# Performance work log

Measured on AMD Instinct MI355X. Metric: run time of the kernel, lower is better.

## Reference

```python
import jax, jax.numpy as jnp
import numpy as np
from jax.scipy.special import logsumexp

B, S, H, T = 64, 512, 768, 9

def setup_inputs() -> dict:
    key = jax.random.key(0)
    ks = jax.random.split(key, 6)
    return {
        "encoder_out": jax.random.normal(ks[0], (B, S, H), jnp.float32),
        "labels": jax.random.randint(ks[1], (B, S), 0, T, jnp.int32),
        "mask": jnp.ones((B, S), jnp.int32),
        "lengths": jnp.full((B,), S, jnp.int32),
        "fc_w": jax.random.normal(ks[2], (T, H), jnp.float32) * 0.02,
        "fc_b": jnp.zeros((T,), jnp.float32),
        "start_trans": jax.random.uniform(ks[3], (T,), jnp.float32, -0.1, 0.1),
        "end_trans": jax.random.uniform(ks[4], (T,), jnp.float32, -0.1, 0.1),
        "trans": jax.random.uniform(ks[5], (T, T), jnp.float32, -0.1, 0.1),
    }

def crf_log_likelihood(em, tg, mk, start, end, trans):
    # em: [S,B,T], tg: [S,B], mk: [S,B] float. torchcrf forward (reduction='none').
    barange = jnp.arange(em.shape[1])
    # --- numerator: score of the gold path ---
    score0 = start[tg[0]] + em[0][barange, tg[0]]
    def num_step(carry, x):
        score, prev = carry
        em_i, tg_i, mk_i = x
        score = score + (trans[prev, tg_i] + em_i[barange, tg_i]) * mk_i
        prev = jnp.where(mk_i > 0, tg_i, prev)
        return (score, prev), None
    (score, prev), _ = jax.lax.scan(num_step, (score0, tg[0]), (em[1:], tg[1:], mk[1:]))
    numerator = score + end[prev]
    # --- denominator: log partition via forward algorithm ---
    alpha = start[None, :] + em[0]  # [B,T]
    def den_step(alpha, x):
        em_i, mk_i = x
        nxt = logsumexp(alpha[:, :, None] + trans[None] + em_i[:, None, :], axis=1)
        return jnp.where(mk_i[:, None] > 0, nxt, alpha), None
    alpha, _ = jax.lax.scan(den_step, alpha, (em[1:], mk[1:]))
    denominator = logsumexp(alpha + end[None, :], axis=1)
    return numerator - denominator  # [B]

def crf_viterbi(em, mk, start, end, trans):
    # em: [S,B,T], mk: [S,B] float. Returns best path [S,B].
    barange = jnp.arange(em.shape[1])
    alpha = start[None, :] + em[0]  # [B,T]
    idT = jnp.arange(em.shape[2])[None, :]
    def fwd_step(alpha, x):
        em_i, mk_i = x
        scores = alpha[:, :, None] + trans[None]  # [B, T_prev, T_cur]
        bp = jnp.argmax(scores, axis=1)           # [B,T]
        nxt = jnp.max(scores, axis=1) + em_i
        valid = mk_i[:, None] > 0
        return jnp.where(valid, nxt, alpha), jnp.where(valid, bp, idT)
    alpha, bps = jax.lax.scan(fwd_step, alpha, (em[1:], mk[1:]))  # bps: [S-1,B,T]
    last = jnp.argmax(alpha + end[None, :], axis=1)  # [B]
    def back_step(tag, bp):
        prev = bp[barange, tag]
        return prev, prev
    _, path_head = jax.lax.scan(back_step, last, bps, reverse=True)  # [S-1,B]
    return jnp.concatenate([path_head, last[None, :]], axis=0)  # [S,B]

def reference(encoder_out, labels, mask, lengths, fc_w, fc_b, start_trans, end_trans, trans):
    # dropout in eval mode == identity
    emissions = jnp.einsum('bsh,th->bst', encoder_out, fc_w) + fc_b  # [B,S,T]
    em = jnp.swapaxes(emissions, 0, 1)               # [S,B,T]
    tg = jnp.swapaxes(labels, 0, 1)                  # [S,B]
    mk = jnp.swapaxes(mask, 0, 1).astype(emissions.dtype)
    ll = crf_log_likelihood(em, tg, mk, start_trans, end_trans, trans)  # [B]
    ner_loss = jnp.mean(-ll)
    path = crf_viterbi(em, mk, start_trans, end_trans, trans)  # [S,B]
    ner_predict = jnp.swapaxes(path, 0, 1)  # [B,S]
    return ner_loss, ner_predict, lengths
```

## Files before the change

### kernel.cpp

```cpp
#include <hip/hip_runtime.h>

#define Bsz 64
#define Ssz 512
#define Hsz 768
#define Tsz 9
#define NCH 16
#define LOG2E 1.4426950408889634f
#define LN2F  0.6931471805599453f
#define PSTR 17

__device__ __forceinline__ int SK(int s) { return s * Tsz + ((s >> 5) << 1); }

__global__ __launch_bounds__(256, 1) void emscan2_kernel(
    const float* __restrict__ x, const float* __restrict__ fcw,
    const float* __restrict__ fcb, const int* __restrict__ mask,
    const float* __restrict__ trans, float* __restrict__ em,
    float* __restrict__ R2, float* __restrict__ MV, int* __restrict__ cnt) {
    __shared__ __align__(16) float4 w4[Tsz * Hsz / 4];
    __shared__ float bias[Tsz];
    __shared__ float part[16 * Tsz * PSTR];
    __shared__ float em_w[33 * Tsz];
    __shared__ int   mk_w[33];
    __shared__ float Elds[81];
    __shared__ float Tlds[81];

    const int tid = threadIdx.x;
    const int bc = blockIdx.x;
    const int b = bc >> 4, c = bc & 15;
    const int base = c * 32;
    const size_t pos0 = (size_t)bc * 32;

    if (bc == 0 && tid == 0) *cnt = 0;

    const float4* fw4 = reinterpret_cast<const float4*>(fcw);
#pragma unroll
    for (int i = 0; i < 7; ++i) {
        const int o = tid + i * 256;
        if (o < 1728) w4[o] = fw4[o];
    }
    if (tid < Tsz) bias[tid] = fcb[tid];
    if (tid >= 16 && tid < 16 + 81) {
        const float t = trans[tid - 16];
        Tlds[tid - 16] = t;
        Elds[tid - 16] = exp2f(t * LOG2E);
    }
    if (tid >= 128 && tid < 128 + 33) {
        const int s = base + (tid - 128);
        mk_w[tid - 128] = (s < Ssz) ? mask[b * Ssz + s] : 0;
    }
    __syncthreads();

    const int p = tid >> 4, l = tid & 15;
    {
        const float4* xr0 = reinterpret_cast<const float4*>(x + (pos0 + p) * Hsz);
        const float4* xr1 = reinterpret_cast<const float4*>(x + (pos0 + 16 + p) * Hsz);
        float acc[Tsz][2];
#pragma unroll
        for (int t = 0; t < Tsz; ++t) { acc[t][0] = 0.0f; acc[t][1] = 0.0f; }
#pragma unroll 4
        for (int i = 0; i < 12; ++i) {
            const float4 xv0 = xr0[i * 16 + l];
            const float4 xv1 = xr1[i * 16 + l];
#pragma unroll
            for (int t = 0; t < Tsz; ++t) {
                const float4 wv = w4[t * 192 + i * 16 + l];
                acc[t][0] = fmaf(xv0.x, wv.x, fmaf(xv0.y, wv.y,
                            fmaf(xv0.z, wv.z, fmaf(xv0.w, wv.w, acc[t][0]))));
                acc[t][1] = fmaf(xv1.x, wv.x, fmaf(xv1.y, wv.y,
                            fmaf(xv1.z, wv.z, fmaf(xv1.w, wv.w, acc[t][1]))));
            }
        }
#pragma unroll
        for (int k = 0; k < 2; ++k) {
            __syncthreads();
#pragma unroll
            for (int t = 0; t < Tsz; ++t) part[(p * Tsz + t) * PSTR + l] = acc[t][k];
            __syncthreads();
            if (tid < 16 * Tsz) {
                const int pq = tid / Tsz, t = tid - pq * Tsz;
                float s = bias[t];
#pragma unroll
                for (int l2 = 0; l2 < 16; ++l2) s += part[(pq * Tsz + t) * PSTR + l2];
                em[(pos0 + (size_t)k * 16 + pq) * Tsz + t] = s;
                em_w[(k * 16 + pq) * Tsz + t] = s;
            }
        }
    }
    if (c < 15) {
        float acc2[Tsz];
#pragma unroll
        for (int t = 0; t < Tsz; ++t) acc2[t] = 0.0f;
        if (tid < 16) {
            const float4* xr2 = reinterpret_cast<const float4*>(x + (pos0 + 32) * Hsz);
#pragma unroll 4
            for (int i = 0; i < 12; ++i) {
                const float4 xv = xr2[i * 16 + l];
#pragma unroll
                for (int t = 0; t < Tsz; ++t) {
                    const float4 wv = w4[t * 192 + i * 16 + l];
                    acc2[t] = fmaf(xv.x, wv.x, fmaf(xv.y, wv.y,
                              fmaf(xv.z, wv.z, fmaf(xv.w, wv.w, acc2[t]))));
                }
            }
        }
        __syncthreads();
        if (tid < 16) {
#pragma unroll
            for (int t = 0; t < Tsz; ++t) part[t * PSTR + l] = acc2[t];
        }
        __syncthreads();
        if (tid < Tsz) {
            float s = bias[tid];
#pragma unroll
            for (int l2 = 0; l2 < 16; ++l2) s += part[tid * PSTR + l2];
            em_w[32 * Tsz + tid] = s;
        }
    }
    __syncthreads();

    const int wv = tid >> 6, ln = tid & 63;
    const int q = ln / 9;
    const int j = ln - q * 9;
    const int tsk = wv * 7 + q;
    if (wv >= 3 || q >= 7 || tsk >= 18) return;
    const int lb = 9 * q;
    const int ns = (c == 15) ? 31 : 32;

    if (tsk < 9) {
        const int a = tsk;
        float Ecol[Tsz];
#pragma unroll
        for (int i = 0; i < Tsz; ++i) Ecol[i] = Elds[i * Tsz + j];
        float pp = (j == a) ? 1.0f : 0.0f;
        float K = 0.0f;
        for (int r = 1; r <= ns; ++r) {
            float g = __shfl(pp, lb, 64) * Ecol[0];
#pragma unroll
            for (int i = 1; i < Tsz; ++i)
                g = fmaf(__shfl(pp, lb + i, 64), Ecol[i], g);
            const float np = g * exp2f(em_w[r * Tsz + j] * LOG2E);
            if (mk_w[r] > 0) pp = np;
            if (((r - 1) & 7) == 7) {
                float ss = __shfl(pp, lb, 64);
#pragma unroll
                for (int i = 1; i < Tsz; ++i) ss += __shfl(pp, lb + i, 64);
                K += __log2f(ss);
                const float inv = 1.0f / ss;
                pp *= inv;
            }
        }
        R2[((size_t)bc * Tsz + a) * Tsz + j] = K + __log2f(pp);
    } else {
        const int a = tsk - 9;
        float Tcol[Tsz];
#pragma unroll
        for (int i = 0; i < Tsz; ++i) Tcol[i] = Tlds[i * Tsz + j];
        float pp = (j == a) ? 0.0f : -1e30f;
        for (int r = 1; r <= ns; ++r) {
            float g = __shfl(pp, lb, 64) + Tcol[0];
#pragma unroll
            for (int i = 1; i < Tsz; ++i)
                g = fmaxf(g, __shfl(pp, lb + i, 64) + Tcol[i]);
            if (mk_w[r] > 0) pp = g + em_w[r * Tsz + j];
        }
        MV[(size_t)bc * 81 + a * Tsz + j] = pp;
    }
}

__device__ __forceinline__ void amax9(const float (&v)[Tsz], float& bv, int& bi) {
    float w01v = (v[1] > v[0]) ? v[1] : v[0]; int w01i = (v[1] > v[0]) ? 1 : 0;
    float w23v = (v[3] > v[2]) ? v[3] : v[2]; int w23i = (v[3] > v[2]) ? 3 : 2;
    float w45v = (v[5] > v[4]) ? v[5] : v[4]; int w45i = (v[5] > v[4]) ? 5 : 4;
    float w67v = (v[7] > v[6]) ? v[7] : v[6]; int w67i = (v[7] > v[6]) ? 7 : 6;
    float x03v = (w23v > w01v) ? w23v : w01v; int x03i = (w23v > w01v) ? w23i : w01i;
    float x47v = (w67v > w45v) ? w67v : w45v; int x47i = (w67v > w45v) ? w67i : w45i;
    float y07v = (x47v > x03v) ? x47v : x03v; int y07i = (x47v > x03v) ? x47i : x03i;
    bv = (v[8] > y07v) ? v[8] : y07v;
    bi = (v[8] > y07v) ? 8 : y07i;
}

__global__ __launch_bounds__(192, 1) void vit3_kernel(
    const float* __restrict__ em, const int* __restrict__ labels,
    const int* __restrict__ mask, const int* __restrict__ lengths,
    const float* __restrict__ start_t, const float* __restrict__ end_t,
    const float* __restrict__ trans, const float* __restrict__ R2,
    const float* __restrict__ MV, float* __restrict__ out_path,
    float* __restrict__ ll, float* __restrict__ dout, int* __restrict__ cnt) {
    __shared__ __align__(16) float em_s[4640];
    __shared__ __align__(16) int   mk_s[Ssz];
    __shared__ __align__(16) float mv_s[NCH * 81];
    __shared__ __align__(16) float r2_s[NCH * 81];
    __shared__ float tr_s[81];
    __shared__ float st_s[12], en_s[12];
    __shared__ __align__(16) float alc[2][NCH][12];
    __shared__ float a2c[2][12];
    __shared__ unsigned char bp[(Ssz - 1) * Tsz];
    __shared__ unsigned char mapA[64][12], mapB[64][12];
    __shared__ float den_sh, num_sh;
    __shared__ int lastf;

    const int b = blockIdx.x, tid = threadIdx.x;
    const int wv = tid >> 6, ln = tid & 63;
    const int c = tid / 12, j9 = tid % 12;
    const float* emb = em + (size_t)b * Ssz * Tsz;
    const int* mkb = mask + b * Ssz;
    const int* lbb = labels + b * Ssz;

    for (int i = tid; i < Ssz * Tsz; i += 192) {
        const int s = i / 9, j = i - s * 9;
        em_s[SK(s) + j] = emb[i];
    }
    for (int i = tid; i < Ssz; i += 192) mk_s[i] = mkb[i];
    {
        const float4* v4 = reinterpret_cast<const float4*>(MV + (size_t)b * NCH * 81);
        float4* vd = reinterpret_cast<float4*>(mv_s);
        for (int i = tid; i < NCH * 81 / 4; i += 192) vd[i] = v4[i];
        const float4* r4 = reinterpret_cast<const float4*>(R2 + (size_t)b * NCH * 81);
        float4* rd = reinterpret_cast<float4*>(r2_s);
        for (int i = tid; i < NCH * 81 / 4; i += 192) rd[i] = r4[i];
        if (tid < 81) tr_s[tid] = trans[tid];
        if (tid >= 96 && tid < 96 + Tsz) {
            st_s[tid - 96] = start_t[tid - 96];
            en_s[tid - 96] = end_t[tid - 96];
        }
    }
    __syncthreads();

    float tc[Tsz];
    const int jj = (j9 < Tsz) ? j9 : Tsz - 1;
#pragma unroll
    for (int i = 0; i < Tsz; ++i) tc[i] = tr_s[i * Tsz + jj];

    float aj = 0.0f;
    if (c == 0 && j9 < Tsz) {
        aj = st_s[j9] + em_s[j9];
        alc[0][0][j9] = aj;
    }
    if (wv == 1 && ln < Tsz) a2c[0][ln] = (st_s[ln] + em_s[ln]) * LOG2E;

    for (int r = 0; r < NCH; ++r) {
        __syncthreads();
        if (r < NCH - 1 && c == r + 1 && j9 < Tsz) {
            const float* M = &mv_s[r * 81];
            float m = alc[0][r][0] + M[j9];
#pragma unroll
            for (int i = 1; i < Tsz; ++i)
                m = fmaxf(m, alc[0][r][i] + M[i * Tsz + j9]);
            aj = m;
            alc[0][c][j9] = m;
        }
        if (wv == 1 && ln < Tsz) {
            const float* Rr = &r2_s[r * 81];
            float xi[Tsz];
#pragma unroll
            for (int i = 0; i < Tsz; ++i) xi[i] = a2c[r & 1][i] + Rr[i * Tsz + ln];
            float m = xi[0];
#pragma unroll
            for (int i = 1; i < Tsz; ++i) m = fmaxf(m, xi[i]);
            float sm = 0.0f;
#pragma unroll
            for (int i = 0; i < Tsz; ++i) sm += exp2f(xi[i] - m);
            a2c[(r + 1) & 1][ln] = m + __log2f(sm);
        }
    }

    int pb = 0;
    for (int k = 0; k < 32; ++k) {
        __syncthreads();
        const int s = c * 32 + 1 + k;
        if (j9 < Tsz && s <= Ssz - 1) {
            const int mk = mk_s[s];
            float av[12];
            const float4* ap = reinterpret_cast<const float4*>(&alc[pb][c][0]);
            *reinterpret_cast<float4*>(&av[0]) = ap[0];
            *reinterpret_cast<float4*>(&av[4]) = ap[1];
            *reinterpret_cast<float4*>(&av[8]) = ap[2];
            float v[Tsz];
#pragma unroll
            for (int i = 0; i < Tsz; ++i) v[i] = av[i] + tc[i];
            float bv; int bi;
            amax9(v, bv, bi);
            bp[(s - 1) * Tsz + j9] = (unsigned char)((mk > 0) ? bi : j9);
            if (mk > 0) aj = bv + em_s[SK(s) + j9];
        }
        if (j9 < Tsz) alc[1 - pb][c][j9] = aj;
        pb ^= 1;
    }
    __syncthreads();

    float bb = alc[0][NCH - 1][0] + en_s[0];
    int last = 0;
#pragma unroll
    for (int q = 1; q < Tsz; ++q) {
        const float qq = alc[0][NCH - 1][q] + en_s[q];
        if (qq > bb) { bb = qq; last = q; }
    }

    const int lo = ln * 8;
    const int hi = min(lo + 7, Ssz - 2);
    if (wv == 0) {
        int xf[Tsz];
#pragma unroll
        for (int t = 0; t < Tsz; ++t) xf[t] = t;
        for (int k = hi; k >= lo; --k) {
#pragma unroll
            for (int t = 0; t < Tsz; ++t) xf[t] = bp[k * Tsz + xf[t]];
        }
#pragma unroll
        for (int t = 0; t < Tsz; ++t) mapA[ln][t] = (unsigned char)xf[t];
    } else if (wv == 1) {
        if (ln == 0) {
            float xv[Tsz];
#pragma unroll
            for (int i = 0; i < Tsz; ++i) xv[i] = a2c[0][i] + en_s[i] * LOG2E;
            float m = xv[0];
#pragma unroll
            for (int i = 1; i < Tsz; ++i) m = fmaxf(m, xv[i]);
            float sm = 0.0f;
#pragma unroll
            for (int i = 0; i < Tsz; ++i) sm += exp2f(xv[i] - m);
            den_sh = m + __log2f(sm);
        }
    } else {
        float part = 0.0f;
        for (int s = 1 + ln; s < Ssz; s += 64) {
            if (mk_s[s] > 0) {
                const int tg = lbb[s];
                int pq = s - 1;
                while (pq > 0 && mk_s[pq] == 0) --pq;
                part += tr_s[lbb[pq] * Tsz + tg] + em_s[SK(s) + tg];
            }
        }
#pragma unroll
        for (int off = 32; off >= 1; off >>= 1) part += __shfl_xor(part, off, 64);
        if (ln == 0) {
            const int tg0 = lbb[0];
            float num = part + st_s[tg0] + em_s[tg0];
            int pq = Ssz - 1;
            while (pq > 0 && mk_s[pq] == 0) --pq;
            num += en_s[lbb[pq]];
            num_sh = num;
        }
    }

#define VIT_RND(CUR, NXT, D)                                               \
    {                                                                      \
        unsigned char nn[Tsz];                                             \
        if (wv == 0) {                                                     \
            const int o = ln + (D);                                        \
            if (o < 64) {                                                  \
                _Pragma("unroll") for (int t = 0; t < Tsz; ++t)            \
                    nn[t] = CUR[ln][CUR[o][t]];                            \
            } else {                                                       \
                _Pragma("unroll") for (int t = 0; t < Tsz; ++t)            \
                    nn[t] = CUR[ln][t];                                    \
            }                                                              \
        }                                                                  \
        __syncthreads();                                                   \
        if (wv == 0) {                                                     \
            _Pragma("unroll") for (int t = 0; t < Tsz; ++t)                \
                NXT[ln][t] = nn[t];                                        \
        }                                                                  \
        __syncthreads();                                                   \
    }
    VIT_RND(mapA, mapB, 1)
    VIT_RND(mapB, mapA, 2)
    VIT_RND(mapA, mapB, 4)
    VIT_RND(mapB, mapA, 8)
    VIT_RND(mapA, mapB, 16)
    VIT_RND(mapB, mapA, 32)
#undef VIT_RND

    if (wv == 0) {
        int t = (ln == 63) ? last : (int)mapA[ln + 1][last];
        float* op = out_path + (size_t)b * Ssz;
        for (int k = hi; k >= lo; --k) {
            t = bp[k * Tsz + t];
            op[k] = (float)t;
        }
        if (ln == 0) op[Ssz - 1] = (float)last;
    }
    if (b == 0 && wv == 2) dout[1 + Bsz * Ssz + ln] = (float)lengths[ln];

    if (tid == 0) {
        ll[b] = num_sh - den_sh * LN2F;
        __threadfence();
        lastf = (atomicAdd(cnt, 1) == Bsz - 1) ? 1 : 0;
    }
    __syncthreads();
    if (lastf && wv == 0) {
        __threadfence();
        float v = ll[ln];
#pragma unroll
        for (int off = 32; off >= 1; off >>= 1) v += __shfl_xor(v, off, 64);
        if (ln == 0) dout[0] = -v * (1.0f / (float)Bsz);
    }
}

extern "C" void kernel_launch(void* const* d_in, const int* in_sizes, int n_in,
                              void* d_out, int out_size, void* d_ws, size_t ws_size,
                              hipStream_t stream) {
    const float* enc    = (const float*)d_in[0];
    const int*   labels = (const int*)d_in[1];
    const int*   mask   = (const int*)d_in[2];
    const int*   lengths= (const int*)d_in[3];
    const float* fcw    = (const float*)d_in[4];
    const float* fcb    = (const float*)d_in[5];
    const float* startt = (const float*)d_in[6];
    const float* endt   = (const float*)d_in[7];
    const float* trans  = (const float*)d_in[8];

    float* out = (float*)d_out;
    float* em  = (float*)d_ws;
    float* R2  = em + (size_t)Bsz * Ssz * Tsz;
    float* MV  = R2 + (size_t)Bsz * NCH * 81;
    float* ll  = MV + (size_t)Bsz * NCH * 81;
    int*   cnt = (int*)(ll + Bsz);

    emscan2_kernel<<<Bsz * NCH, 256, 0, stream>>>(enc, fcw, fcb, mask, trans,
                                                  em, R2, MV, cnt);
    vit3_kernel<<<Bsz, 192, 0, stream>>>(em, labels, mask, lengths, startt, endt,
                                         trans, R2, MV, out + 1, ll, out, cnt);
}
```

Before: 71.03 us.

## Use wavefront shuffle reductions and software-pipelined loads in emission GEMV kernel

Replaces the shared-memory partial-sum buffer and its two barrier rounds with __shfl_xor reductions across the 16 lanes that share a position. The x loads are manually double-buffered so the next two float4 chunks are fetched while the current ones are multiplied. Launch bounds are raised from 1 to 4 blocks per CU so more blocks can be resident. These changes target barrier stalls and memory latency, at the cost of more register pressure from the prefetched values, which may limit the occupancy actually reached.

```diff
diff --git a/kernel.cpp b/kernel.cpp
--- a/kernel.cpp
+++ b/kernel.cpp
@@ -7,18 +7,20 @@
 #define NCH 16
 #define LOG2E 1.4426950408889634f
 #define LN2F  0.6931471805599453f
-#define PSTR 17
 
 __device__ __forceinline__ int SK(int s) { return s * Tsz + ((s >> 5) << 1); }
 
-__global__ __launch_bounds__(256, 1) void emscan2_kernel(
+#define FMA4(ACC, V, W)                                                    \
+    ACC = fmaf((V).x, (W).x, fmaf((V).y, (W).y,                            \
+          fmaf((V).z, (W).z, fmaf((V).w, (W).w, (ACC)))))
+
+__global__ __launch_bounds__(256, 4) void emscan3_kernel(
     const float* __restrict__ x, const float* __restrict__ fcw,
     const float* __restrict__ fcb, const int* __restrict__ mask,
     const float* __restrict__ trans, float* __restrict__ em,
     float* __restrict__ R2, float* __restrict__ MV, int* __restrict__ cnt) {
     __shared__ __align__(16) float4 w4[Tsz * Hsz / 4];
     __shared__ float bias[Tsz];
-    __shared__ float part[16 * Tsz * PSTR];
     __shared__ float em_w[33 * Tsz];
     __shared__ int   mk_w[33];
     __shared__ float Elds[81];
@@ -39,82 +41,116 @@
         if (o < 1728) w4[o] = fw4[o];
     }
     if (tid < Tsz) bias[tid] = fcb[tid];
-    if (tid >= 16 && tid < 16 + 81) {
+    if (tid >= 16 && tid < 97) {
         const float t = trans[tid - 16];
         Tlds[tid - 16] = t;
         Elds[tid - 16] = exp2f(t * LOG2E);
     }
-    if (tid >= 128 && tid < 128 + 33) {
+    if (tid >= 128 && tid < 161) {
         const int s = base + (tid - 128);
         mk_w[tid - 128] = (s < Ssz) ? mask[b * Ssz + s] : 0;
     }
     __syncthreads();
 
     const int p = tid >> 4, l = tid & 15;
+
     {
         const float4* xr0 = reinterpret_cast<const float4*>(x + (pos0 + p) * Hsz);
         const float4* xr1 = reinterpret_cast<const float4*>(x + (pos0 + 16 + p) * Hsz);
-        float acc[Tsz][2];
-#pragma unroll
-        for (int t = 0; t < Tsz; ++t) { acc[t][0] = 0.0f; acc[t][1] = 0.0f; }
-#pragma unroll 4
-        for (int i = 0; i < 12; ++i) {
-            const float4 xv0 = xr0[i * 16 + l];
-            const float4 xv1 = xr1[i * 16 + l];
-#pragma unroll
-            for (int t = 0; t < Tsz; ++t) {
-                const float4 wv = w4[t * 192 + i * 16 + l];
-                acc[t][0] = fmaf(xv0.x, wv.x, fmaf(xv0.y, wv.y,
-                            fmaf(xv0.z, wv.z, fmaf(xv0.w, wv.w, acc[t][0]))));
-                acc[t][1] = fmaf(xv1.x, wv.x, fmaf(xv1.y, wv.y,
-                            fmaf(xv1.z, wv.z, fmaf(xv1.w, wv.w, acc[t][1]))));
-            }
-        }
-#pragma unroll
-        for (int k = 0; k < 2; ++k) {
-            __syncthreads();
-#pragma unroll
-            for (int t = 0; t < Tsz; ++t) part[(p * Tsz + t) * PSTR + l] = acc[t][k];
-            __syncthreads();
-            if (tid < 16 * Tsz) {
-                const int pq = tid / Tsz, t = tid - pq * Tsz;
-                float s = bias[t];
-#pragma unroll
-                for (int l2 = 0; l2 < 16; ++l2) s += part[(pq * Tsz + t) * PSTR + l2];
-                em[(pos0 + (size_t)k * 16 + pq) * Tsz + t] = s;
-                em_w[(k * 16 + pq) * Tsz + t] = s;
-            }
-        }
-    }
-    if (c < 15) {
+        float acc0[Tsz], acc1[Tsz];
+#pragma unroll
+        for (int t = 0; t < Tsz; ++t) { acc0[t] = 0.0f; acc1[t] = 0.0f; }
+
+        float4 A0, A1, A2, A3, B0, B1, B2, B3;
+#define FMAP(V0, V1, V2, V3, I)                                            \
+        _Pragma("unroll") for (int t = 0; t < Tsz; ++t) {                  \
+            const float4 w0 = w4[t * 192 + (I) * 16 + l];                  \
+            const float4 w1 = w4[t * 192 + ((I) + 1) * 16 + l];            \
+            FMA4(acc0[t], V0, w0); FMA4(acc1[t], V1, w0);                  \
+            FMA4(acc0[t], V2, w1); FMA4(acc1[t], V3, w1);                  \
+        }
+        A0 = xr0[0 * 16 + l];  A1 = xr1[0 * 16 + l];
+        A2 = xr0[1 * 16 + l];  A3 = xr1[1 * 16 + l];
+        B0 = xr0[2 * 16 + l];  B1 = xr1[2 * 16 + l];
+        B2 = xr0[3 * 16 + l];  B3 = xr1[3 * 16 + l];
+        FMAP(A0, A1, A2, A3, 0)
+        A0 = xr0[4 * 16 + l];  A1 = xr1[4 * 16 + l];
+        A2 = xr0[5 * 16 + l];  A3 = xr1[5 * 16 + l];
+        FMAP(B0, B1, B2, B3, 2)
+        B0 = xr0[6 * 16 + l];  B1 = xr1[6 * 16 + l];
+        B2 = xr0[7 * 16 + l];  B3 = xr1[7 * 16 + l];
+        FMAP(A0, A1, A2, A3, 4)
+        A0 = xr0[8 * 16 + l];  A1 = xr1[8 * 16 + l];
+        A2 = xr0[9 * 16 + l];  A3 = xr1[9 * 16 + l];
+        FMAP(B0, B1, B2, B3, 6)
+        B0 = xr0[10 * 16 + l]; B1 = xr1[10 * 16 + l];
+        B2 = xr0[11 * 16 + l]; B3 = xr1[11 * 16 + l];
+        FMAP(A0, A1, A2, A3, 8)
+        FMAP(B0, B1, B2, B3, 10)
+#undef FMAP
+
+#pragma unroll
+        for (int t = 0; t < Tsz; ++t) {
+            acc0[t] += __shfl_xor(acc0[t], 1, 64);
+            acc0[t] += __shfl_xor(acc0[t], 2, 64);
+            acc0[t] += __shfl_xor(acc0[t], 4, 64);
+            acc0[t] += __shfl_xor(acc0[t], 8, 64);
+            acc1[t] += __shfl_xor(acc1[t], 1, 64);
+            acc1[t] += __shfl_xor(acc1[t], 2, 64);
+            acc1[t] += __shfl_xor(acc1[t], 4, 64);
+            acc1[t] += __shfl_xor(acc1[t], 8, 64);
+        }
+        float o0 = 0.0f, o1 = 0.0f;
+#pragma unroll
+        for (int t = 0; t < Tsz; ++t)
+            if (l == t) { o0 = acc0[t]; o1 = acc1[t]; }
+        if (l < Tsz) {
+            const float bse = bias[l];
+            const float v0 = o0 + bse, v1 = o1 + bse;
+            em[(pos0 + p) * Tsz + l] = v0;
+            em_w[p * Tsz + l] = v0;
+            em[(pos0 + 16 + p) * Tsz + l] = v1;
+            em_w[(16 + p) * Tsz + l] = v1;
+        }
+    }
+
+    if (c < 15 && tid < 16) {
+        const float4* xr2 = reinterpret_cast<const float4*>(x + (pos0 + 32) * Hsz);
         float acc2[Tsz];
 #pragma unroll
         for (int t = 0; t < Tsz; ++t) acc2[t] = 0.0f;
-        if (tid < 16) {
-            const float4* xr2 = reinterpret_cast<const float4*>(x + (pos0 + 32) * Hsz);
-#pragma unroll 4
-            for (int i = 0; i < 12; ++i) {
-                const float4 xv = xr2[i * 16 + l];
-#pragma unroll
-                for (int t = 0; t < Tsz; ++t) {
-                    const float4 wv = w4[t * 192 + i * 16 + l];
-                    acc2[t] = fmaf(xv.x, wv.x, fmaf(xv.y, wv.y,
-                              fmaf(xv.z, wv.z, fmaf(xv.w, wv.w, acc2[t]))));
-                }
-            }
-        }
-        __syncthreads();
-        if (tid < 16) {
-#pragma unroll
-            for (int t = 0; t < Tsz; ++t) part[t * PSTR + l] = acc2[t];
-        }
-        __syncthreads();
-        if (tid < Tsz) {
-            float s = bias[tid];
-#pragma unroll
-            for (int l2 = 0; l2 < 16; ++l2) s += part[tid * PSTR + l2];
-            em_w[32 * Tsz + tid] = s;
-        }
+        float4 A0, A2, B0, B2;
+#define FMAS(V0, V2, I)                                                    \
+        _Pragma("unroll") for (int t = 0; t < Tsz; ++t) {                  \
+            const float4 w0 = w4[t * 192 + (I) * 16 + l];                  \
+            const float4 w1 = w4[t * 192 + ((I) + 1) * 16 + l];            \
+            FMA4(acc2[t], V0, w0); FMA4(acc2[t], V2, w1);                  \
+        }
+        A0 = xr2[0 * 16 + l];  A2 = xr2[1 * 16 + l];
+        B0 = xr2[2 * 16 + l];  B2 = xr2[3 * 16 + l];
+        FMAS(A0, A2, 0)
+        A0 = xr2[4 * 16 + l];  A2 = xr2[5 * 16 + l];
+        FMAS(B0, B2, 2)
+        B0 = xr2[6 * 16 + l];  B2 = xr2[7 * 16 + l];
+        FMAS(A0, A2, 4)
+        A0 = xr2[8 * 16 + l];  A2 = xr2[9 * 16 + l];
+        FMAS(B0, B2, 6)
+        B0 = xr2[10 * 16 + l]; B2 = xr2[11 * 16 + l];
+        FMAS(A0, A2, 8)
+        FMAS(B0, B2, 10)
+#undef FMAS
+#pragma unroll
+        for (int t = 0; t < Tsz; ++t) {
+            acc2[t] += __shfl_xor(acc2[t], 1, 64);
+            acc2[t] += __shfl_xor(acc2[t], 2, 64);
+            acc2[t] += __shfl_xor(acc2[t], 4, 64);
+            acc2[t] += __shfl_xor(acc2[t], 8, 64);
+        }
+        float o2 = 0.0f;
+#pragma unroll
+        for (int t = 0; t < Tsz; ++t)
+            if (l == t) o2 = acc2[t];
+        if (l < Tsz) em_w[32 * Tsz + l] = o2 + bias[l];
     }
     __syncthreads();
 
@@ -417,7 +453,7 @@
     float* ll  = MV + (size_t)Bsz * NCH * 81;
     int*   cnt = (int*)(ll + Bsz);
 
-    emscan2_kernel<<<Bsz * NCH, 256, 0, stream>>>(enc, fcw, fcb, mask, trans,
+    emscan3_kernel<<<Bsz * NCH, 256, 0, stream>>>(enc, fcw, fcb, mask, trans,
                                                   em, R2, MV, cnt);
     vit3_kernel<<<Bsz, 192, 0, stream>>>(em, labels, mask, lengths, startt, endt,
                                          trans, R2, MV, out + 1, ll, out, cnt);
```

After: 69.01 us. 1.03x faster.
